# Optimization experiments

Measured on AMD Instinct MI355X. Metric: run time of the kernel, lower is better.

Reference implementation:

```python
import jax, jax.numpy as jnp
import numpy as np

N = 100000      # nodes
E = 1600000     # edges
DIN, DH, DOUT = 128, 256, 40


def setup_inputs() -> dict:
    key = jax.random.key(0)
    ks = jax.random.split(key, 24)

    def w(i, fan_in, fan_out):
        s = 1.0 / np.sqrt(fan_in)
        return jax.random.uniform(ks[i], (fan_in, fan_out), jnp.float32, -s, s)

    def b(i, fan_in, fan_out):
        s = 1.0 / np.sqrt(fan_in)
        return jax.random.uniform(ks[i], (fan_out,), jnp.float32, -s, s)

    return {
        "x": jax.random.normal(ks[0], (N, DIN), jnp.float32),
        "edge_index": jax.random.randint(ks[1], (2, E), 0, N, dtype=jnp.int64),
        # updates_continues: Linear(DIN,DH), Linear(DH,DH), Linear(DH,DOUT)
        "Wc0": w(2, DIN, DH),  "bc0": b(3, DIN, DH),
        "Wc1": w(4, DH, DH),   "bc1": b(5, DH, DH),
        "Wc2": w(6, DH, DOUT), "bc2": b(7, DH, DOUT),
        # updates_exit: Linear(DIN,DOUT) x2, Linear(DH,DOUT) x2
        "We0": w(8, DIN, DOUT),  "be0": b(9, DIN, DOUT),
        "We1": w(10, DIN, DOUT), "be1": b(11, DIN, DOUT),
        "We2": w(12, DH, DOUT),  "be2": b(13, DH, DOUT),
        "We3": w(14, DH, DOUT),  "be3": b(15, DH, DOUT),
    }


def _gcn_agg(h, src, dst):
    """Symmetric-normalized GCN aggregation with self-loops: D^-1/2 (A+I) D^-1/2 h."""
    ones = jnp.ones(src.shape[0], h.dtype)
    deg = jax.ops.segment_sum(ones, dst, num_segments=N) + 1.0  # self-loop
    dinv = jax.lax.rsqrt(deg)
    coef = dinv[src] * dinv[dst]                    # [E]
    msgs = h[src] * coef[:, None]                   # [E, d] gather
    out = jax.ops.segment_sum(msgs, dst, num_segments=N)  # scatter-add
    return out + h * (dinv * dinv)[:, None]         # self-loop term


def reference(x, edge_index, Wc0, bc0, Wc1, bc1, Wc2, bc2,
              We0, be0, We1, be1, We2, be2, We3, be3):
    src, dst = edge_index[0], edge_index[1]
    Wc = [(Wc0, bc0), (Wc1, bc1), (Wc2, bc2)]
    We = [(We0, be0), (We1, be1), (We2, be2), (We3, be3)]

    h = x
    outs = [jax.nn.log_softmax(h @ We[0][0] + We[0][1], axis=1)]
    for i in range(3):
        h = _gcn_agg(h, src, dst)
        outs.append(jax.nn.log_softmax(h @ We[i + 1][0] + We[i + 1][1], axis=1))
        h = h @ Wc[i][0] + Wc[i][1]
        if i < 2:
            h = jax.nn.relu(h)  # dropout is identity in eval mode
    return jnp.stack(outs, axis=1)  # [N, num_layers+1, DOUT]
```

## Files before the change

kernel.cpp:

```cpp
#include <hip/hip_runtime.h>

#define NNODES 100000
#define NEDGES 1600000

typedef __attribute__((ext_vector_type(8))) short bf16x8;
typedef __attribute__((ext_vector_type(4))) float f32x4;

__device__ __forceinline__ float bf2f(unsigned v) {
  union { unsigned u; float f; } x; x.u = v << 16; return x.f;
}
__device__ __forceinline__ unsigned short f2bf(float f) {
  union { float f; unsigned u; } x; x.f = f;
  unsigned r = x.u + 0x7fffu + ((x.u >> 16) & 1u);
  return (unsigned short)(r >> 16);
}

__global__ void k_probe(const unsigned* __restrict__ xw, const int* __restrict__ ei,
                        int* __restrict__ flags) {
  __shared__ int cF, cI;
  if (threadIdx.x == 0) { cF = 0; cI = 0; }
  __syncthreads();
  int t = threadIdx.x;
  int hf = 0;
  for (int i = t; i < 2048; i += 256) {
    unsigned lo = xw[i] & 0xffffu;
    unsigned e = (lo >> 7) & 0xffu;
    if (e >= 0xC0u) hf++;
  }
  atomicAdd(&cF, hf);
  int hi = 0;
  if (ei[2 * t + 1] != 0) hi++;
  atomicAdd(&cI, hi);
  __syncthreads();
  if (threadIdx.x == 0) {
    flags[0] = (cF > 32) ? 1 : 0;
    flags[1] = (cI < 16) ? 1 : 0;
  }
}

__device__ __forceinline__ int edge_at(const int* __restrict__ ei, int j, int i64) {
  return i64 ? ei[2 * j] : ei[j];
}

struct CvtParams {
  const void* src[13];
  unsigned short* dst[13];
  int n[13];
};

__global__ void k_cvt(CvtParams p, const int* __restrict__ flags) {
  int a = blockIdx.y;
  int n = p.n[a];
  int f32 = flags[0];
  const float* sf = (const float*)p.src[a];
  const unsigned short* sb = (const unsigned short*)p.src[a];
  unsigned short* d = p.dst[a];
  for (int i = blockIdx.x * blockDim.x + threadIdx.x; i < n; i += gridDim.x * blockDim.x) {
    d[i] = f32 ? f2bf(sf[i]) : sb[i];
  }
}

__global__ void k_transpose(const unsigned short* __restrict__ W,
                            unsigned short* __restrict__ WT, int K) {
  int idx = blockIdx.x * 256 + threadIdx.x;
  if (idx < K * 256) {
    int k = idx >> 8, c = idx & 255;
    WT[c * K + k] = W[idx];
  }
}

template <int K>
__global__ void k_transpose40(const unsigned short* __restrict__ W,
                              unsigned short* __restrict__ WT) {
  int idx = blockIdx.x * 256 + threadIdx.x;
  if (idx < 48 * K) {
    int c = idx / K, k = idx % K;
    WT[idx] = (c < 40) ? W[k * 40 + c] : (unsigned short)0;
  }
}

__global__ void k_zero(int* __restrict__ p, int n) {
  int v = blockIdx.x * blockDim.x + threadIdx.x;
  if (v < n) p[v] = 0;
}

__global__ void k_count(const int* __restrict__ ei, int* __restrict__ cnt,
                        const int* __restrict__ flags) {
  int e = blockIdx.x * blockDim.x + threadIdx.x;
  if (e < NEDGES) {
    int i64 = flags[1];
    int d = edge_at(ei, NEDGES + e, i64);
    if ((unsigned)d < NNODES) atomicAdd(&cnt[d], 1);
  }
}

__global__ void k_dinv(const int* __restrict__ cnt, float* __restrict__ dinv) {
  int v = blockIdx.x * blockDim.x + threadIdx.x;
  if (v < NNODES) dinv[v] = rsqrtf((float)cnt[v] + 1.0f);
}

__global__ void k_psum(const int* __restrict__ cnt, int* __restrict__ bsum) {
  __shared__ int sw[4];
  int t = threadIdx.x;
  int i = blockIdx.x * 256 + t;
  int v = (i < NNODES) ? cnt[i] : 0;
  int x = v;
#pragma unroll
  for (int o = 1; o < 64; o <<= 1) {
    int y = __shfl_up(x, o, 64);
    if ((t & 63) >= o) x += y;
  }
  if ((t & 63) == 63) sw[t >> 6] = x;
  __syncthreads();
  if (t == 0) bsum[blockIdx.x] = sw[0] + sw[1] + sw[2] + sw[3];
}

__global__ void k_bscan(const int* __restrict__ bsum, int* __restrict__ bbase,
                        int* __restrict__ offs) {
  int l = threadIdx.x;
  int base = l * 7;
  int v[7];
  int s = 0;
#pragma unroll
  for (int k = 0; k < 7; ++k) {
    int j = base + k;
    v[k] = (j < 391) ? bsum[j] : 0;
    s += v[k];
  }
  int x = s;
#pragma unroll
  for (int o = 1; o < 64; o <<= 1) {
    int y = __shfl_up(x, o, 64);
    if (l >= o) x += y;
  }
  int excl = x - s;
#pragma unroll
  for (int k = 0; k < 7; ++k) {
    int j = base + k;
    if (j < 391) bbase[j] = excl;
    excl += v[k];
  }
  if (l == 63) offs[NNODES] = x;
}

__global__ void k_offs(const int* __restrict__ cnt, const int* __restrict__ bbase,
                       int* __restrict__ offs, int* __restrict__ cursor) {
  __shared__ int sw[4], swo[4];
  int t = threadIdx.x;
  int i = blockIdx.x * 256 + t;
  int v = (i < NNODES) ? cnt[i] : 0;
  int x = v;
#pragma unroll
  for (int o = 1; o < 64; o <<= 1) {
    int y = __shfl_up(x, o, 64);
    if ((t & 63) >= o) x += y;
  }
  if ((t & 63) == 63) sw[t >> 6] = x;
  __syncthreads();
  if (t == 0) {
    int a = 0;
#pragma unroll
    for (int w = 0; w < 4; ++w) { swo[w] = a; a += sw[w]; }
  }
  __syncthreads();
  if (i < NNODES) {
    int e = bbase[blockIdx.x] + swo[t >> 6] + x - v;
    offs[i] = e;
    cursor[i] = e;
  }
}

__global__ void k_fill(const int* __restrict__ ei, int* __restrict__ cursor,
                       int* __restrict__ csr_src, const int* __restrict__ flags) {
  int e = blockIdx.x * blockDim.x + threadIdx.x;
  if (e < NEDGES) {
    int i64 = flags[1];
    int s = edge_at(ei, e, i64), d = edge_at(ei, NEDGES + e, i64);
    if ((unsigned)s < NNODES && (unsigned)d < NNODES) {
      int p = atomicAdd(&cursor[d], 1);
      if ((unsigned)p < NEDGES) csr_src[p] = s;
    }
  }
}

__device__ __forceinline__ void acc8(float (&acc)[8], uint4 u, float w) {
  acc[0] += w * bf2f(u.x & 0xffffu);
  acc[1] += w * bf2f(u.x >> 16);
  acc[2] += w * bf2f(u.y & 0xffffu);
  acc[3] += w * bf2f(u.y >> 16);
  acc[4] += w * bf2f(u.z & 0xffffu);
  acc[5] += w * bf2f(u.z >> 16);
  acc[6] += w * bf2f(u.w & 0xffffu);
  acc[7] += w * bf2f(u.w >> 16);
}

template <int D, bool GDINV>
__global__ __launch_bounds__(256) void k_agg(
    const unsigned short* __restrict__ hin, unsigned short* __restrict__ hout,
    const int* __restrict__ offs, const int* __restrict__ csr_src,
    const float* __restrict__ dinv) {
  constexpr int LPR = D / 8;
  constexpr int R = 64 / LPR;
  constexpr int NB = 8 / R;
  const int lane = threadIdx.x & 63;
  const int g = lane / LPR;
  const int l = lane % LPR;
  const int v = (blockIdx.x * 256 + threadIdx.x) >> 6;
  if (v >= NNODES) return;

  float dv = dinv[v];
  const size_t vbase = (size_t)v * D + l * 8;
  uint4 su = *(const uint4*)(hin + vbase);
  float acc[8];
#pragma unroll
  for (int k = 0; k < 8; ++k) acc[k] = 0.f;
  acc8(acc, su, (g == 0) ? (GDINV ? dv : 1.f) : 0.f);

  int b0 = offs[v];
  int n = offs[v + 1] - b0;
  for (int i = 0; i < n; i += 8) {
    int s[NB];
    float wg[NB];
#pragma unroll
    for (int j = 0; j < NB; ++j) {
      int ei = i + j * R + g;
      int ec = (ei < n) ? ei : (n - 1);
      s[j] = csr_src[b0 + ec];
      wg[j] = (ei < n) ? (GDINV ? dinv[s[j]] : 1.f) : 0.f;
    }
    uint4 gu[NB];
#pragma unroll
    for (int j = 0; j < NB; ++j)
      gu[j] = *(const uint4*)(hin + (size_t)s[j] * D + l * 8);
#pragma unroll
    for (int j = 0; j < NB; ++j) acc8(acc, gu[j], wg[j]);
  }
#pragma unroll
  for (int k = 0; k < 8; ++k) {
#pragma unroll
    for (int o = LPR; o < 64; o <<= 1) acc[k] += __shfl_xor(acc[k], o, 64);
  }
  if (g == 0) {
    uint4 ov;
    ov.x = (unsigned)f2bf(dv * acc[0]) | ((unsigned)f2bf(dv * acc[1]) << 16);
    ov.y = (unsigned)f2bf(dv * acc[2]) | ((unsigned)f2bf(dv * acc[3]) << 16);
    ov.z = (unsigned)f2bf(dv * acc[4]) | ((unsigned)f2bf(dv * acc[5]) << 16);
    ov.w = (unsigned)f2bf(dv * acc[6]) | ((unsigned)f2bf(dv * acc[7]) << 16);
    *(uint4*)(hout + vbase) = ov;
  }
}

__global__ __launch_bounds__(256) void k_agg40(
    const unsigned short* __restrict__ P, const int* __restrict__ offs,
    const int* __restrict__ csr_src, const float* __restrict__ dinv,
    const unsigned short* __restrict__ bias, float* __restrict__ outp) {
  const int lane = threadIdx.x & 63;
  const int g = lane >> 5, l = lane & 31;
  const bool act = l < 20;
  const int v = (blockIdx.x * 256 + threadIdx.x) >> 6;
  if (v >= NNODES) return;

  float dv = dinv[v];
  float a0 = 0.f, a1 = 0.f;
  if (act && g == 0) {
    unsigned su = *(const unsigned*)(P + (size_t)v * 40 + l * 2);
    a0 = bf2f(su & 0xffffu);
    a1 = bf2f(su >> 16);
  }
  int b0 = offs[v];
  int n = offs[v + 1] - b0;
  for (int i = 0; i < n; i += 8) {
    int s[4];
    float wg[4];
#pragma unroll
    for (int j = 0; j < 4; ++j) {
      int ei = i + j * 2 + g;
      int ec = (ei < n) ? ei : (n - 1);
      s[j] = csr_src[b0 + ec];
      wg[j] = (ei < n) ? 1.f : 0.f;
    }
    unsigned gu[4];
#pragma unroll
    for (int j = 0; j < 4; ++j)
      gu[j] = act ? *(const unsigned*)(P + (size_t)s[j] * 40 + l * 2) : 0u;
#pragma unroll
    for (int j = 0; j < 4; ++j) {
      a0 += wg[j] * bf2f(gu[j] & 0xffffu);
      a1 += wg[j] * bf2f(gu[j] >> 16);
    }
  }
  a0 += __shfl_xor(a0, 32, 64);
  a1 += __shfl_xor(a1, 32, 64);
  if (act) {
    a0 = dv * a0 + bf2f((unsigned)bias[l * 2]);
    a1 = dv * a1 + bf2f((unsigned)bias[l * 2 + 1]);
  }
  float m = act ? fmaxf(a0, a1) : -1e30f;
#pragma unroll
  for (int o = 16; o > 0; o >>= 1) m = fmaxf(m, __shfl_xor(m, o, 32));
  float ss = act ? (expf(a0 - m) + expf(a1 - m)) : 0.f;
#pragma unroll
  for (int o = 16; o > 0; o >>= 1) ss += __shfl_xor(ss, o, 32);
  float ls = logf(ss) + m;
  if (act && g == 0) {
    float2 o2;
    o2.x = a0 - ls;
    o2.y = a1 - ls;
    *(float2*)(outp + (size_t)v * 160 + l * 2) = o2;
  }
}

template <int K, bool SCALE>
__global__ __launch_bounds__(256) void k_mlp_mfma(
    const unsigned short* __restrict__ A, const unsigned short* __restrict__ WT,
    const unsigned short* __restrict__ bias, unsigned short* __restrict__ out,
    const float* __restrict__ dinv) {
  __shared__ short As[128 * 40];
  __shared__ short Bs[128 * 40];
  const int t = threadIdx.x;
  const int lane = t & 63, wv = t >> 6;
  const int m0 = blockIdx.x * 128;
  const int c0 = blockIdx.y * 128;
  const int mw = (wv >> 1) * 64, nw = (wv & 1) * 64;
  const int lr = lane & 15, lq = lane >> 4;

  f32x4 acc[4][4];
#pragma unroll
  for (int i = 0; i < 4; ++i)
#pragma unroll
    for (int j = 0; j < 4; ++j) acc[i][j] = (f32x4)0.f;

  for (int kc = 0; kc < K; kc += 32) {
    __syncthreads();
#pragma unroll
    for (int it = 0; it < 2; ++it) {
      int idx = t + it * 256;
      int row = idx >> 2, seg = idx & 3;
      uint4 u = make_uint4(0, 0, 0, 0);
      int gr = m0 + row;
      if (gr < NNODES) u = *(const uint4*)(A + (size_t)gr * K + kc + seg * 8);
      *(uint4*)&As[row * 40 + seg * 8] = u;
      uint4 v = *(const uint4*)(WT + (size_t)(c0 + row) * K + kc + seg * 8);
      *(uint4*)&Bs[row * 40 + seg * 8] = v;
    }
    __syncthreads();
    bf16x8 af[4], bfr[4];
#pragma unroll
    for (int i = 0; i < 4; ++i)
      af[i] = *(const bf16x8*)&As[(mw + 16 * i + lr) * 40 + lq * 8];
#pragma unroll
    for (int j = 0; j < 4; ++j)
      bfr[j] = *(const bf16x8*)&Bs[(nw + 16 * j + lr) * 40 + lq * 8];
#pragma unroll
    for (int i = 0; i < 4; ++i)
#pragma unroll
      for (int j = 0; j < 4; ++j)
        acc[i][j] = __builtin_amdgcn_mfma_f32_16x16x32_bf16(af[i], bfr[j], acc[i][j], 0, 0, 0);
  }

  float bv[4];
#pragma unroll
  for (int j = 0; j < 4; ++j) bv[j] = bf2f((unsigned)bias[c0 + nw + 16 * j + lr]);
#pragma unroll
  for (int i = 0; i < 4; ++i) {
    int rbase = m0 + mw + 16 * i + lq * 4;
#pragma unroll
    for (int r = 0; r < 4; ++r) {
      int row = rbase + r;
      if (row < NNODES) {
        float s = SCALE ? dinv[row] : 1.f;
#pragma unroll
        for (int j = 0; j < 4; ++j) {
          int col = c0 + nw + 16 * j + lr;
          float v = fmaxf(acc[i][j][r] + bv[j], 0.f) * s;
          out[(size_t)row * 256 + col] = f2bf(v);
        }
      }
    }
  }
}

template <int K, bool SOFTMAX>
__global__ __launch_bounds__(256) void k_exit_mfma(
    const unsigned short* __restrict__ A, const unsigned short* __restrict__ WT,
    const unsigned short* __restrict__ bias, float* __restrict__ outp,
    unsigned short* __restrict__ Pout, const float* __restrict__ dinv) {
  constexpr int KP = K + 8;
  __shared__ short As[128 * 40];
  __shared__ short Bs[48 * KP];
  const int t = threadIdx.x;
  const int lane = t & 63, wv = t >> 6;
  const int m0 = blockIdx.x * 128;
  const int mw = wv * 32;
  const int lr = lane & 15, lq = lane >> 4;

  for (int idx = t; idx < 48 * (K / 8); idx += 256) {
    int row = idx / (K / 8), seg = idx % (K / 8);
    uint4 w = *(const uint4*)(WT + (size_t)row * K + seg * 8);
    *(uint4*)&Bs[row * KP + seg * 8] = w;
  }

  f32x4 acc[2][3];
#pragma unroll
  for (int i = 0; i < 2; ++i)
#pragma unroll
    for (int j = 0; j < 3; ++j) acc[i][j] = (f32x4)0.f;

  for (int kc = 0; kc < K; kc += 32) {
    __syncthreads();
#pragma unroll
    for (int it = 0; it < 2; ++it) {
      int idx = t + it * 256;
      int row = idx >> 2, seg = idx & 3;
      uint4 u = make_uint4(0, 0, 0, 0);
      int gr = m0 + row;
      if (gr < NNODES) u = *(const uint4*)(A + (size_t)gr * K + kc + seg * 8);
      *(uint4*)&As[row * 40 + seg * 8] = u;
    }
    __syncthreads();
    bf16x8 af[2], bfr[3];
#pragma unroll
    for (int i = 0; i < 2; ++i)
      af[i] = *(const bf16x8*)&As[(mw + 16 * i + lr) * 40 + lq * 8];
#pragma unroll
    for (int j = 0; j < 3; ++j)
      bfr[j] = *(const bf16x8*)&Bs[(16 * j + lr) * KP + kc + lq * 8];
#pragma unroll
    for (int i = 0; i < 2; ++i)
#pragma unroll
      for (int j = 0; j < 3; ++j)
        acc[i][j] = __builtin_amdgcn_mfma_f32_16x16x32_bf16(af[i], bfr[j], acc[i][j], 0, 0, 0);
  }

  if (SOFTMAX) {
    float bv0 = bf2f((unsigned)bias[lr]);
    float bv1 = bf2f((unsigned)bias[16 + lr]);
    float bv2 = (lr < 8) ? bf2f((unsigned)bias[32 + lr]) : 0.f;
#pragma unroll
    for (int i = 0; i < 2; ++i) {
#pragma unroll
      for (int r = 0; r < 4; ++r) {
        int row = m0 + mw + 16 * i + lq * 4 + r;
        float v0 = acc[i][0][r] + bv0;
        float v1 = acc[i][1][r] + bv1;
        float v2 = (lr < 8) ? (acc[i][2][r] + bv2) : -1e30f;
        float m = fmaxf(fmaxf(v0, v1), v2);
#pragma unroll
        for (int o = 8; o > 0; o >>= 1) m = fmaxf(m, __shfl_xor(m, o, 16));
        float ss = expf(v0 - m) + expf(v1 - m) + ((lr < 8) ? expf(v2 - m) : 0.f);
#pragma unroll
        for (int o = 8; o > 0; o >>= 1) ss += __shfl_xor(ss, o, 16);
        float ls = logf(ss) + m;
        if (row < NNODES) {
          outp[(size_t)row * 160 + lr] = v0 - ls;
          outp[(size_t)row * 160 + 16 + lr] = v1 - ls;
          if (lr < 8) outp[(size_t)row * 160 + 32 + lr] = v2 - ls;
        }
      }
    }
  } else {
#pragma unroll
    for (int i = 0; i < 2; ++i) {
#pragma unroll
      for (int r = 0; r < 4; ++r) {
        int row = m0 + mw + 16 * i + lq * 4 + r;
        if (row < NNODES) {
          float s = dinv[row];
          Pout[(size_t)row * 40 + lr] = f2bf(acc[i][0][r] * s);
          Pout[(size_t)row * 40 + 16 + lr] = f2bf(acc[i][1][r] * s);
          if (lr < 8) Pout[(size_t)row * 40 + 32 + lr] = f2bf(acc[i][2][r] * s);
        }
      }
    }
  }
}

extern "C" void kernel_launch(void* const* d_in, const int* in_sizes, int n_in,
                              void* d_out, int out_size, void* d_ws, size_t ws_size,
                              hipStream_t stream) {
  const void* x_raw   = d_in[0];
  const int* ei       = (const int*)d_in[1];
  float* out          = (float*)d_out;

  char* ws = (char*)d_ws;
  int*   flags    = (int*)(ws + 0);
  int*   bsum     = (int*)(ws + 1024);
  int*   bbase    = (int*)(ws + 2816);
  int*   cnt      = (int*)(ws + 8192);
  int*   offs     = (int*)(ws + 524288);
  int*   cursor   = (int*)(ws + 1048576);
  float* dinv     = (float*)(ws + 1572864);
  int*   csr_src  = (int*)(ws + 2097152);
  unsigned short* xb = (unsigned short*)(ws + 16777216);
  unsigned short* wb = (unsigned short*)(ws + 45088768);
  unsigned short* hA = (unsigned short*)(ws + 48234496);
  unsigned short* hB = (unsigned short*)(ws + 100663296);
  unsigned short* P  = xb;

  unsigned short* Wc0 = wb + 0;
  unsigned short* bc0 = wb + 32768;
  unsigned short* Wc1 = wb + 33024;
  unsigned short* bc1 = wb + 98560;
  unsigned short* We0 = wb + 98816;
  unsigned short* be0 = wb + 103936;
  unsigned short* We1 = wb + 103976;
  unsigned short* be1 = wb + 109096;
  unsigned short* We2 = wb + 109136;
  unsigned short* be2 = wb + 119376;
  unsigned short* We3 = wb + 119416;
  unsigned short* be3 = wb + 129656;
  unsigned short* WTc0  = wb + 131072;
  unsigned short* WTc1  = wb + 163840;
  unsigned short* WT40e0 = wb + 229376;
  unsigned short* WT40e1 = wb + 235520;
  unsigned short* WT40e2 = wb + 241664;
  unsigned short* WT40e3 = wb + 253952;

  dim3 B(256);
  k_probe<<<dim3(1), B, 0, stream>>>((const unsigned*)x_raw, ei, flags);
  k_zero<<<dim3(391), B, 0, stream>>>(cnt, NNODES);

  CvtParams p;
  const int srcIdx[13] = {0, 2, 3, 4, 5, 8, 9, 10, 11, 12, 13, 14, 15};
  unsigned short* dsts[13] = {xb, Wc0, bc0, Wc1, bc1, We0, be0, We1, be1, We2, be2, We3, be3};
  const int ns[13] = {NNODES * 128, 128 * 256, 256, 256 * 256, 256,
                      128 * 40, 40, 128 * 40, 40, 256 * 40, 40, 256 * 40, 40};
  for (int i = 0; i < 13; ++i) { p.src[i] = d_in[srcIdx[i]]; p.dst[i] = dsts[i]; p.n[i] = ns[i]; }
  k_cvt<<<dim3(1024, 13), B, 0, stream>>>(p, flags);
  k_transpose<<<dim3(128), B, 0, stream>>>(Wc0, WTc0, 128);
  k_transpose<<<dim3(256), B, 0, stream>>>(Wc1, WTc1, 256);
  k_transpose40<128><<<dim3(24), B, 0, stream>>>(We0, WT40e0);
  k_transpose40<128><<<dim3(24), B, 0, stream>>>(We1, WT40e1);
  k_transpose40<256><<<dim3(48), B, 0, stream>>>(We2, WT40e2);
  k_transpose40<256><<<dim3(48), B, 0, stream>>>(We3, WT40e3);

  k_count<<<dim3(6250), B, 0, stream>>>(ei, cnt, flags);
  k_dinv<<<dim3(391), B, 0, stream>>>(cnt, dinv);
  k_psum<<<dim3(391), B, 0, stream>>>(cnt, bsum);
  k_bscan<<<dim3(1), dim3(64), 0, stream>>>(bsum, bbase, offs);
  k_offs<<<dim3(391), B, 0, stream>>>(cnt, bbase, offs, cursor);
  k_fill<<<dim3(6250), B, 0, stream>>>(ei, cursor, csr_src, flags);

  k_exit_mfma<128, true><<<dim3(782), B, 0, stream>>>(xb, WT40e0, be0, out + 0 * 40, nullptr, dinv);
  k_agg<128, true><<<dim3(25000), B, 0, stream>>>(xb, hA, offs, csr_src, dinv);
  k_exit_mfma<128, true><<<dim3(782), B, 0, stream>>>(hA, WT40e1, be1, out + 1 * 40, nullptr, dinv);
  k_mlp_mfma<128, true><<<dim3(782, 2), B, 0, stream>>>(hA, WTc0, bc0, hB, dinv);
  k_agg<256, false><<<dim3(25000), B, 0, stream>>>(hB, hA, offs, csr_src, dinv);
  k_exit_mfma<256, true><<<dim3(782), B, 0, stream>>>(hA, WT40e2, be2, out + 2 * 40, nullptr, dinv);
  k_mlp_mfma<256, false><<<dim3(782, 2), B, 0, stream>>>(hA, WTc1, bc1, hB, nullptr);
  k_exit_mfma<256, false><<<dim3(782), B, 0, stream>>>(hB, WT40e3, nullptr, nullptr, P, dinv);
  k_agg40<<<dim3(25000), B, 0, stream>>>(P, offs, csr_src, dinv, be3, out + 3 * 40);
}
```

Baseline: 770.3 us.

## Build CSR via two-level bucketed counting sort with shared-memory histograms

Replaces the per-node global-atomic CSR construction (count, dinv, psum, bscan, offs, fill) with a two-pass bucket sort. Edges are first histogrammed into 782 buckets of 128 destination nodes using LDS atomics, then staged as packed (local dst, src) records, and finally each bucket is placed into CSR order by one block using LDS atomics. This is meant to cut the heavily contended global atomics and the scattered writes of the old fill pass. In exchange it adds an extra staging buffer and a second read of the edge list, and packing src into 17 bits only fits node counts up to 131072.

```diff
diff --git a/kernel.cpp b/kernel.cpp
--- a/kernel.cpp
+++ b/kernel.cpp
@@ -2,6 +2,7 @@
 
 #define NNODES 100000
 #define NEDGES 1600000
+#define NBKT 782
 
 typedef __attribute__((ext_vector_type(8))) short bf16x8;
 typedef __attribute__((ext_vector_type(4))) float f32x4;
@@ -84,47 +85,38 @@
   if (v < n) p[v] = 0;
 }
 
-__global__ void k_count(const int* __restrict__ ei, int* __restrict__ cnt,
-                        const int* __restrict__ flags) {
-  int e = blockIdx.x * blockDim.x + threadIdx.x;
-  if (e < NEDGES) {
-    int i64 = flags[1];
-    int d = edge_at(ei, NEDGES + e, i64);
-    if ((unsigned)d < NNODES) atomicAdd(&cnt[d], 1);
-  }
-}
-
-__global__ void k_dinv(const int* __restrict__ cnt, float* __restrict__ dinv) {
-  int v = blockIdx.x * blockDim.x + threadIdx.x;
-  if (v < NNODES) dinv[v] = rsqrtf((float)cnt[v] + 1.0f);
-}
-
-__global__ void k_psum(const int* __restrict__ cnt, int* __restrict__ bsum) {
-  __shared__ int sw[4];
+
+__global__ __launch_bounds__(256) void k_bcnt(const int* __restrict__ ei,
+                                              int* __restrict__ bcnt,
+                                              const int* __restrict__ flags) {
+  __shared__ int h[NBKT];
   int t = threadIdx.x;
-  int i = blockIdx.x * 256 + t;
-  int v = (i < NNODES) ? cnt[i] : 0;
-  int x = v;
-#pragma unroll
-  for (int o = 1; o < 64; o <<= 1) {
-    int y = __shfl_up(x, o, 64);
-    if ((t & 63) >= o) x += y;
-  }
-  if ((t & 63) == 63) sw[t >> 6] = x;
-  __syncthreads();
-  if (t == 0) bsum[blockIdx.x] = sw[0] + sw[1] + sw[2] + sw[3];
-}
-
-__global__ void k_bscan(const int* __restrict__ bsum, int* __restrict__ bbase,
-                        int* __restrict__ offs) {
+  for (int i = t; i < NBKT; i += 256) h[i] = 0;
+  __syncthreads();
+  int i64 = flags[1];
+  int e0 = blockIdx.x * 4096;
+#pragma unroll
+  for (int k = 0; k < 16; ++k) {
+    int e = e0 + t + k * 256;
+    if (e < NEDGES) {
+      int d = edge_at(ei, NEDGES + e, i64);
+      if ((unsigned)d < NNODES) atomicAdd(&h[d >> 7], 1);
+    }
+  }
+  __syncthreads();
+  for (int i = t; i < NBKT; i += 256)
+    if (h[i]) atomicAdd(&bcnt[i], h[i]);
+}
+
+__global__ void k_bscan2(const int* __restrict__ bcnt, int* __restrict__ bbase,
+                         int* __restrict__ gcur) {
   int l = threadIdx.x;
-  int base = l * 7;
-  int v[7];
+  int v[13];
   int s = 0;
 #pragma unroll
-  for (int k = 0; k < 7; ++k) {
-    int j = base + k;
-    v[k] = (j < 391) ? bsum[j] : 0;
+  for (int k = 0; k < 13; ++k) {
+    int j = l * 13 + k;
+    v[k] = (j < NBKT) ? bcnt[j] : 0;
     s += v[k];
   }
   int x = s;
@@ -135,51 +127,97 @@
   }
   int excl = x - s;
 #pragma unroll
-  for (int k = 0; k < 7; ++k) {
-    int j = base + k;
-    if (j < 391) bbase[j] = excl;
+  for (int k = 0; k < 13; ++k) {
+    int j = l * 13 + k;
+    if (j < NBKT) { bbase[j] = excl; gcur[j] = excl; }
     excl += v[k];
   }
-  if (l == 63) offs[NNODES] = x;
-}
-
-__global__ void k_offs(const int* __restrict__ cnt, const int* __restrict__ bbase,
-                       int* __restrict__ offs, int* __restrict__ cursor) {
-  __shared__ int sw[4], swo[4];
+  if (l == 63) bbase[NBKT] = x;
+}
+
+__global__ __launch_bounds__(256) void k_bstage(const int* __restrict__ ei,
+                                                int* __restrict__ gcur,
+                                                int* __restrict__ stage,
+                                                const int* __restrict__ flags) {
+  __shared__ int h[NBKT];
+  __shared__ int base[NBKT];
   int t = threadIdx.x;
-  int i = blockIdx.x * 256 + t;
-  int v = (i < NNODES) ? cnt[i] : 0;
-  int x = v;
-#pragma unroll
-  for (int o = 1; o < 64; o <<= 1) {
-    int y = __shfl_up(x, o, 64);
-    if ((t & 63) >= o) x += y;
-  }
-  if ((t & 63) == 63) sw[t >> 6] = x;
-  __syncthreads();
-  if (t == 0) {
-    int a = 0;
-#pragma unroll
-    for (int w = 0; w < 4; ++w) { swo[w] = a; a += sw[w]; }
-  }
-  __syncthreads();
-  if (i < NNODES) {
-    int e = bbase[blockIdx.x] + swo[t >> 6] + x - v;
-    offs[i] = e;
-    cursor[i] = e;
-  }
-}
-
-__global__ void k_fill(const int* __restrict__ ei, int* __restrict__ cursor,
-                       int* __restrict__ csr_src, const int* __restrict__ flags) {
-  int e = blockIdx.x * blockDim.x + threadIdx.x;
-  if (e < NEDGES) {
-    int i64 = flags[1];
-    int s = edge_at(ei, e, i64), d = edge_at(ei, NEDGES + e, i64);
-    if ((unsigned)s < NNODES && (unsigned)d < NNODES) {
-      int p = atomicAdd(&cursor[d], 1);
-      if ((unsigned)p < NEDGES) csr_src[p] = s;
-    }
+  for (int i = t; i < NBKT; i += 256) h[i] = 0;
+  __syncthreads();
+  int i64 = flags[1];
+  int e0 = blockIdx.x * 4096;
+  int bkt[16], lp[16], rec[16];
+#pragma unroll
+  for (int k = 0; k < 16; ++k) {
+    bkt[k] = -1;
+    int e = e0 + t + k * 256;
+    if (e < NEDGES) {
+      int d = edge_at(ei, NEDGES + e, i64);
+      if ((unsigned)d < NNODES) {
+        int s = edge_at(ei, e, i64);
+        if ((unsigned)s >= NNODES) s = NNODES - 1;
+        bkt[k] = d >> 7;
+        rec[k] = ((d & 127) << 17) | s;
+        lp[k] = atomicAdd(&h[bkt[k]], 1);
+      }
+    }
+  }
+  __syncthreads();
+  for (int i = t; i < NBKT; i += 256)
+    base[i] = h[i] ? atomicAdd(&gcur[i], h[i]) : 0;
+  __syncthreads();
+#pragma unroll
+  for (int k = 0; k < 16; ++k)
+    if (bkt[k] >= 0) stage[base[bkt[k]] + lp[k]] = rec[k];
+}
+
+__global__ __launch_bounds__(256) void k_bplace(const int* __restrict__ stage,
+                                                const int* __restrict__ bbase,
+                                                int* __restrict__ offs,
+                                                float* __restrict__ dinv,
+                                                int* __restrict__ csr_src) {
+  __shared__ int h[128];
+  __shared__ int cur[128];
+  int b = blockIdx.x;
+  int t = threadIdx.x;
+  int n0 = b * 128;
+  int NN = NNODES - n0; if (NN > 128) NN = 128;
+  int s0 = bbase[b], s1 = bbase[b + 1];
+  int cnt = s1 - s0;
+  if (t < 128) h[t] = 0;
+  __syncthreads();
+  for (int i = t; i < cnt; i += 256) {
+    int rec = stage[s0 + i];
+    atomicAdd(&h[rec >> 17], 1);
+  }
+  __syncthreads();
+  if (t < 64) {
+    int a = h[2 * t], c = h[2 * t + 1];
+    int s = a + c;
+    int x = s;
+#pragma unroll
+    for (int o = 1; o < 64; o <<= 1) {
+      int y = __shfl_up(x, o, 64);
+      if (t >= o) x += y;
+    }
+    int excl = s0 + x - s;
+    cur[2 * t] = excl;
+    cur[2 * t + 1] = excl + a;
+    if (2 * t < NN) {
+      offs[n0 + 2 * t] = excl;
+      dinv[n0 + 2 * t] = rsqrtf((float)a + 1.0f);
+    }
+    if (2 * t + 1 < NN) {
+      offs[n0 + 2 * t + 1] = excl + a;
+      dinv[n0 + 2 * t + 1] = rsqrtf((float)c + 1.0f);
+    }
+  }
+  if (b == NBKT - 1 && t == 0) offs[NNODES] = s1;
+  __syncthreads();
+  for (int i = t; i < cnt; i += 256) {
+    int rec = stage[s0 + i];
+    int pos = atomicAdd(&cur[rec >> 17], 1);
+    csr_src[pos] = rec & 0x1FFFF;
   }
 }
 
@@ -484,13 +522,13 @@
 
   char* ws = (char*)d_ws;
   int*   flags    = (int*)(ws + 0);
-  int*   bsum     = (int*)(ws + 1024);
-  int*   bbase    = (int*)(ws + 2816);
-  int*   cnt      = (int*)(ws + 8192);
-  int*   offs     = (int*)(ws + 524288);
-  int*   cursor   = (int*)(ws + 1048576);
-  float* dinv     = (float*)(ws + 1572864);
+  int*   bcnt     = (int*)(ws + 4096);
+  int*   gcur     = (int*)(ws + 8192);
+  int*   bbase    = (int*)(ws + 12288);
+  float* dinv     = (float*)(ws + 524288);
+  int*   offs     = (int*)(ws + 1048576);
   int*   csr_src  = (int*)(ws + 2097152);
+  int*   stage    = (int*)(ws + 8650752);
   unsigned short* xb = (unsigned short*)(ws + 16777216);
   unsigned short* wb = (unsigned short*)(ws + 45088768);
   unsigned short* hA = (unsigned short*)(ws + 48234496);
@@ -518,7 +556,7 @@
 
   dim3 B(256);
   k_probe<<<dim3(1), B, 0, stream>>>((const unsigned*)x_raw, ei, flags);
-  k_zero<<<dim3(391), B, 0, stream>>>(cnt, NNODES);
+  k_zero<<<dim3(4), B, 0, stream>>>(bcnt, NBKT);
 
   CvtParams p;
   const int srcIdx[13] = {0, 2, 3, 4, 5, 8, 9, 10, 11, 12, 13, 14, 15};
@@ -534,12 +572,10 @@
   k_transpose40<256><<<dim3(48), B, 0, stream>>>(We2, WT40e2);
   k_transpose40<256><<<dim3(48), B, 0, stream>>>(We3, WT40e3);
 
-  k_count<<<dim3(6250), B, 0, stream>>>(ei, cnt, flags);
-  k_dinv<<<dim3(391), B, 0, stream>>>(cnt, dinv);
-  k_psum<<<dim3(391), B, 0, stream>>>(cnt, bsum);
-  k_bscan<<<dim3(1), dim3(64), 0, stream>>>(bsum, bbase, offs);
-  k_offs<<<dim3(391), B, 0, stream>>>(cnt, bbase, offs, cursor);
-  k_fill<<<dim3(6250), B, 0, stream>>>(ei, cursor, csr_src, flags);
+  k_bcnt<<<dim3(391), B, 0, stream>>>(ei, bcnt, flags);
+  k_bscan2<<<dim3(1), dim3(64), 0, stream>>>(bcnt, bbase, gcur);
+  k_bstage<<<dim3(391), B, 0, stream>>>(ei, gcur, stage, flags);
+  k_bplace<<<dim3(NBKT), B, 0, stream>>>(stage, bbase, offs, dinv, csr_src);
 
   k_exit_mfma<128, true><<<dim3(782), B, 0, stream>>>(xb, WT40e0, be0, out + 0 * 40, nullptr, dinv);
   k_agg<128, true><<<dim3(25000), B, 0, stream>>>(xb, hA, offs, csr_src, dinv);
```

Measured after the change: 630.4 us. 18.2% less time.
